# Kernel optimization log

Measured on AMD Instinct MI355X. Metric: run time of the kernel, lower is better.

Reference implementation:

```python
import jax, jax.numpy as jnp
import numpy as np
from functools import partial

B, T_DEC, S_ENC = 64, 30, 31
E, U, V = 128, 256, 32000

def setup_inputs() -> dict:
    key = jax.random.key(0)
    ks = jax.random.split(key, 12)
    sc = lambda *s: 1.0 / np.sqrt(s[0])
    return {
        "inputs": jax.random.randint(ks[0], (B, T_DEC), 0, V, dtype=jnp.int64),
        "memory": jax.random.normal(ks[1], (B, S_ENC, U), jnp.float32),
        "sample_h": jax.random.normal(ks[2], (B, U), jnp.float32),
        "sample_c": jax.random.normal(ks[3], (B, U), jnp.float32),
        "emb_table": jax.random.normal(ks[4], (V, E), jnp.float32) * 0.02,
        "W_k": jax.random.normal(ks[5], (E + U, 4 * U), jnp.float32) * sc(E + U),
        "W_r": jax.random.normal(ks[6], (U, 4 * U), jnp.float32) * sc(U),
        "b_lstm": jnp.zeros((4 * U,), jnp.float32),
        "W_mem": jax.random.normal(ks[7], (U, U), jnp.float32) * sc(U),
        "W_attn": jax.random.normal(ks[8], (2 * U, U), jnp.float32) * sc(2 * U),
        "W_fc": jax.random.normal(ks[9], (U, V), jnp.float32) * sc(U),
        "b_fc": jnp.zeros((V,), jnp.float32),
    }

def _decode(inputs, memory, sample_h, sample_c, emb_table, W_k, W_r, b_lstm,
            W_mem, W_attn, W_fc, b_fc):
    # Luong attention keys: memory_layer(memory), no bias. [B,S,U]
    keys = jnp.einsum('bsu,uv->bsv', memory, W_mem)
    x_emb = emb_table[inputs]                       # [B,T,E]
    xs = jnp.swapaxes(x_emb, 0, 1)                  # [T,B,E]

    def step(carry, x_t):
        h, c, attn = carry
        # AttentionWrapper cell_input_fn: concat(input, prev_attention)
        cell_in = jnp.concatenate([x_t, attn], axis=-1)           # [B,E+U]
        z = cell_in @ W_k + h @ W_r + b_lstm                      # [B,4U]
        i, f, g, o = jnp.split(z, 4, axis=-1)
        c = jax.nn.sigmoid(f) * c + jax.nn.sigmoid(i) * jnp.tanh(g)
        h = jax.nn.sigmoid(o) * jnp.tanh(c)
        # Luong score: query . keys ; memory_sequence_length covers all S, no mask
        score = jnp.einsum('bu,bsu->bs', h, keys)                 # [B,S]
        align = jax.nn.softmax(score, axis=-1)
        context = jnp.einsum('bs,bsu->bu', align, memory)         # [B,U]
        # attention_layer: Dense(U, use_bias=False) on concat(cell_out, context)
        attn = jnp.concatenate([h, context], axis=-1) @ W_attn    # [B,U]
        out_t = attn @ W_fc + b_fc                                # [B,V]
        return (h, c, attn), out_t

    init = (sample_h, sample_c, jnp.zeros((sample_h.shape[0], U), sample_h.dtype))
    _, outs = jax.lax.scan(step, init, xs)          # [T,B,V]
    return jnp.swapaxes(outs, 0, 1)                 # [B,T,V]

def reference(inputs, memory, sample_h, sample_c, emb_table, W_k, W_r, b_lstm,
              W_mem, W_attn, W_fc, b_fc):
    return _decode(inputs, memory, sample_h, sample_c, emb_table, W_k, W_r,
                   b_lstm, W_mem, W_attn, W_fc, b_fc)
```

## Files before the change

kernel.cpp:

```cpp
#include <hip/hip_runtime.h>
#include <hip/hip_bf16.h>
#include <math.h>

constexpr int NB = 64;
constexpr int NT = 30;
constexpr int NS = 31;
constexpr int NE = 128;
constexpr int NU = 256;
constexpr int NV = 32000;
constexpr int NG = 4 * NU;

__device__ __forceinline__ float sigmoidf_(float x) {
    return 1.0f / (1.0f + __expf(-x));
}

__global__ __launch_bounds__(256) void keys_kernel(
    const float* __restrict__ memory, const float* __restrict__ W_mem,
    float* __restrict__ keys) {
    const int row0 = blockIdx.x * 8;
    const int u = threadIdx.x;
    __shared__ float mS[8][NU];
#pragma unroll
    for (int r = 0; r < 8; ++r) mS[r][u] = memory[(row0 + r) * NU + u];
    __syncthreads();
    float acc[8] = {0, 0, 0, 0, 0, 0, 0, 0};
#pragma unroll 4
    for (int v = 0; v < NU; ++v) {
        float w = W_mem[v * NU + u];
#pragma unroll
        for (int r = 0; r < 8; ++r) acc[r] += mS[r][v] * w;
    }
#pragma unroll
    for (int r = 0; r < 8; ++r) keys[(row0 + r) * NU + u] = acc[r];
}

__global__ __launch_bounds__(256) void fuse_wz_kernel(
    const float* __restrict__ W_k,
    const float* __restrict__ W_r,
    const float* __restrict__ W_a,
    float* __restrict__ Wzp)
{
    const int col = blockIdx.x * 256 + threadIdx.x;
    const int rb = blockIdx.y * 8;
    __shared__ float waS[8][NU];
#pragma unroll
    for (int r = 0; r < 8; ++r) waS[r][threadIdx.x] = W_a[(size_t)(rb + r) * NU + threadIdx.x];
    __syncthreads();
    float acc[8] = {};
#pragma unroll 4
    for (int j = 0; j < NU; ++j) {
        float w = W_k[(size_t)(NE + j) * NG + col];
#pragma unroll
        for (int r = 0; r < 8; ++r) acc[r] += waS[r][j] * w;
    }
    const int gate = col >> 8, u = col & 255;
    const int qb = u >> 6, lc = gate * 64 + (u & 63);
#pragma unroll
    for (int r = 0; r < 8; ++r) {
        int i = rb + r;
        float v = acc[r];
        if (i < NU) v += W_r[(size_t)i * NG + col];
        Wzp[(size_t)qb * 512 * 256 + (size_t)i * 256 + lc] = v;
    }
}

__global__ __launch_bounds__(256) void zemb_kernel(
    const int* __restrict__ inputs, const float* __restrict__ emb,
    const float* __restrict__ W_k, const float* __restrict__ b_lstm,
    float* __restrict__ z_emb)
{
    const int col = blockIdx.x * 256 + threadIdx.x;
    const int m0 = blockIdx.y * 8;
    __shared__ float eS[8][NE];
    for (int i = threadIdx.x; i < 8 * NE; i += 256) {
        int r = i >> 7, e = i & 127;
        eS[r][e] = emb[(size_t)inputs[m0 + r] * NE + e];
    }
    __syncthreads();
    float acc[8] = {};
#pragma unroll 4
    for (int e = 0; e < NE; ++e) {
        float w = W_k[(size_t)e * NG + col];
#pragma unroll
        for (int r = 0; r < 8; ++r) acc[r] += eS[r][e] * w;
    }
    float bb = b_lstm[col];
#pragma unroll
    for (int r = 0; r < 8; ++r) z_emb[(size_t)(m0 + r) * NG + col] = acc[r] + bb;
}

__global__ __launch_bounds__(1024, 4) void recurrence_coop(
    const float* __restrict__ z_emb,
    const float* __restrict__ sample_h,
    const float* __restrict__ sample_c,
    const float* __restrict__ Wzp,
    const float* __restrict__ W_r,
    const float* __restrict__ memory,
    const float* __restrict__ keys,
    float* __restrict__ h_all,
    float* __restrict__ ctx_all,
    unsigned* __restrict__ bar)
{
    const int bid = blockIdx.x;
    const int b  = bid & 63;
    const int qb = bid >> 6;
    const int tid = threadIdx.x;

    __shared__ float memS[NS * NU];
    __shared__ float zPart[16 * 256];
    __shared__ float actS[2 * NU];
    __shared__ float scS[32];

    const float* memb = memory + (size_t)b * NS * NU;
    const float* keyb = keys + (size_t)b * NS * NU;
    for (int i = tid; i < NS * NU / 4; i += 1024)
        ((float4*)memS)[i] = ((const float4*)memb)[i];
    if (tid < NU) actS[tid] = sample_h[b * NU + tid];
    float c_reg = (tid < 64) ? sample_c[b * NU + qb * 64 + tid] : 0.0f;

    const int colq = tid & 63;
    const int p    = tid >> 6;
    const int gate = colq >> 4, wq = colq & 15;
    const int ncol = gate * 256 + qb * 64 + wq * 4;
    const float* panel = Wzp + (size_t)qb * 512 * 256;
    const float* zerow = z_emb + (size_t)(b * NT) * NG + ncol;
    unsigned* ctr = bar + b;

    __syncthreads();

    for (int t = 0; t < NT; ++t) {
        {
            float4 acc = (p == 0) ? *(const float4*)(zerow + (size_t)t * NG)
                                  : make_float4(0.f, 0.f, 0.f, 0.f);
            if (t == 0) {
                const float* ap = actS + p * 16;
#pragma unroll
                for (int k = 0; k < 16; ++k) {
                    float a = ap[k];
                    float4 w = *(const float4*)(W_r + (size_t)(p * 16 + k) * NG + ncol);
                    acc.x += a * w.x; acc.y += a * w.y;
                    acc.z += a * w.z; acc.w += a * w.w;
                }
            } else {
                const float* ap = actS + p * 32;
                const float* wp = panel + (size_t)(p * 32) * 256 + colq * 4;
#pragma unroll 8
                for (int k = 0; k < 32; ++k) {
                    float a = ap[k];
                    float4 w = *(const float4*)(wp + k * 256);
                    acc.x += a * w.x; acc.y += a * w.y;
                    acc.z += a * w.z; acc.w += a * w.w;
                }
            }
            *(float4*)(zPart + p * 256 + colq * 4) = acc;
        }
        __syncthreads();

        const size_t m = (size_t)b * NT + t;
        if (tid < 64) {
            float zv[4];
#pragma unroll
            for (int g = 0; g < 4; ++g) {
                float s = 0.f;
#pragma unroll
                for (int q = 0; q < 16; ++q) s += zPart[q * 256 + g * 64 + tid];
                zv[g] = s;
            }
            c_reg = sigmoidf_(zv[1]) * c_reg + sigmoidf_(zv[0]) * tanhf(zv[2]);
            float h = sigmoidf_(zv[3]) * tanhf(c_reg);
            __hip_atomic_store(h_all + m * NU + qb * 64 + tid, h,
                               __ATOMIC_RELAXED, __HIP_MEMORY_SCOPE_AGENT);
        }
        __syncthreads();

        if (tid == 0) {
            __hip_atomic_fetch_add(ctr, 1u, __ATOMIC_RELAXED,
                                   __HIP_MEMORY_SCOPE_AGENT);
            const unsigned tgt = 4u * (unsigned)(t + 1);
            while (__hip_atomic_load(ctr, __ATOMIC_RELAXED,
                                     __HIP_MEMORY_SCOPE_AGENT) < tgt)
                __builtin_amdgcn_s_sleep(2);
        }
        __syncthreads();

        if (tid < NU)
            actS[tid] = __hip_atomic_load(h_all + m * NU + tid,
                                          __ATOMIC_RELAXED,
                                          __HIP_MEMORY_SCOPE_AGENT);
        __syncthreads();

        {
            const int s = tid >> 5, j = tid & 31;
            if (s < NS) {
                float sp = 0.0f;
#pragma unroll
                for (int i = 0; i < 8; ++i)
                    sp += actS[i * 32 + j] * keyb[s * NU + i * 32 + j];
#pragma unroll
                for (int msk = 16; msk; msk >>= 1) sp += __shfl_xor(sp, msk, 32);
                if (j == 0) scS[s] = sp;
            }
        }
        __syncthreads();

        if (tid < NU) {
            float mx = scS[0];
#pragma unroll
            for (int s = 1; s < NS; ++s) mx = fmaxf(mx, scS[s]);
            float sumE = 0.0f, ctx = 0.0f;
#pragma unroll 4
            for (int s = 0; s < NS; ++s) {
                float e = __expf(scS[s] - mx);
                sumE += e;
                ctx += e * memS[s * NU + tid];
            }
            ctx /= sumE;
            actS[NU + tid] = ctx;
            if (qb == 0) ctx_all[m * NU + tid] = ctx;
        }
        __syncthreads();
    }
}

__global__ __launch_bounds__(256) void attn_kernel(
    const float* __restrict__ h_all, const float* __restrict__ ctx_all,
    const float* __restrict__ W_a, float* __restrict__ attn_all)
{
    const int j = threadIdx.x;
    const int m0 = blockIdx.x * 8;
    __shared__ float hS[8][NU], cS[8][NU];
    for (int i = j; i < 8 * NU; i += 256) {
        int r = i >> 8, k = i & 255;
        hS[r][k] = h_all[(size_t)(m0 + r) * NU + k];
        cS[r][k] = ctx_all[(size_t)(m0 + r) * NU + k];
    }
    __syncthreads();
    float acc[8] = {};
#pragma unroll 2
    for (int k = 0; k < NU; ++k) {
        float w1 = W_a[(size_t)k * NU + j];
        float w2 = W_a[(size_t)(NU + k) * NU + j];
#pragma unroll
        for (int r = 0; r < 8; ++r) acc[r] += hS[r][k] * w1 + cS[r][k] * w2;
    }
#pragma unroll
    for (int r = 0; r < 8; ++r) attn_all[(size_t)(m0 + r) * NU + j] = acc[r];
}

constexpr int BM = 128, BN = 128, KC = 32, KTOT = NU;

__global__ __launch_bounds__(256) void out_gemm(
    const float* __restrict__ A,
    const float* __restrict__ Wfc,
    const float* __restrict__ bfc,
    float* __restrict__ out)
{
    const int n0 = blockIdx.x * BN;
    const int m0 = blockIdx.y * BM;
    const int tid = threadIdx.x;
    const int tx = tid & 15, ty = tid >> 4;

    __shared__ float As[KC][BM + 4];
    __shared__ float Bs[KC][BN];

    float acc[2][4][2][4] = {};

    const int kq = tid & 7,  r0 = tid >> 3;
    const int nq = tid & 31, kr0 = tid >> 5;

    float4 aR[4], bR[4];

#pragma unroll
    for (int p = 0; p < 4; ++p)
        aR[p] = *(const float4*)(A + (size_t)(m0 + r0 + p * 32) * KTOT + kq * 4);
#pragma unroll
    for (int p = 0; p < 4; ++p)
        bR[p] = *(const float4*)(Wfc + (size_t)(kr0 + p * 8) * NV + n0 + nq * 4);
#pragma unroll
    for (int p = 0; p < 4; ++p) {
        int r = r0 + p * 32;
        As[kq * 4 + 0][r] = aR[p].x;
        As[kq * 4 + 1][r] = aR[p].y;
        As[kq * 4 + 2][r] = aR[p].z;
        As[kq * 4 + 3][r] = aR[p].w;
        *(float4*)&Bs[kr0 + p * 8][nq * 4] = bR[p];
    }
    __syncthreads();

    for (int kb = 0; kb < KTOT; kb += KC) {
        const bool more = (kb + KC) < KTOT;
        if (more) {
#pragma unroll
            for (int p = 0; p < 4; ++p)
                aR[p] = *(const float4*)(A + (size_t)(m0 + r0 + p * 32) * KTOT + kb + KC + kq * 4);
#pragma unroll
            for (int p = 0; p < 4; ++p)
                bR[p] = *(const float4*)(Wfc + (size_t)(kb + KC + kr0 + p * 8) * NV + n0 + nq * 4);
        }

#pragma unroll 4
        for (int k = 0; k < KC; ++k) {
            float4 a0 = *(const float4*)&As[k][ty * 4];
            float4 a1 = *(const float4*)&As[k][64 + ty * 4];
            float4 b0 = *(const float4*)&Bs[k][tx * 4];
            float4 b1 = *(const float4*)&Bs[k][64 + tx * 4];
            float am[2][4] = {{a0.x, a0.y, a0.z, a0.w}, {a1.x, a1.y, a1.z, a1.w}};
            float bv[2][4] = {{b0.x, b0.y, b0.z, b0.w}, {b1.x, b1.y, b1.z, b1.w}};
#pragma unroll
            for (int im = 0; im < 2; ++im)
#pragma unroll
                for (int i = 0; i < 4; ++i)
#pragma unroll
                    for (int jn = 0; jn < 2; ++jn)
#pragma unroll
                        for (int j = 0; j < 4; ++j)
                            acc[im][i][jn][j] += am[im][i] * bv[jn][j];
        }
        __syncthreads();

        if (more) {
#pragma unroll
            for (int p = 0; p < 4; ++p) {
                int r = r0 + p * 32;
                As[kq * 4 + 0][r] = aR[p].x;
                As[kq * 4 + 1][r] = aR[p].y;
                As[kq * 4 + 2][r] = aR[p].z;
                As[kq * 4 + 3][r] = aR[p].w;
                *(float4*)&Bs[kr0 + p * 8][nq * 4] = bR[p];
            }
            __syncthreads();
        }
    }

    float4 bias[2];
    bias[0] = *(const float4*)(bfc + n0 + tx * 4);
    bias[1] = *(const float4*)(bfc + n0 + 64 + tx * 4);
#pragma unroll
    for (int im = 0; im < 2; ++im)
#pragma unroll
        for (int i = 0; i < 4; ++i) {
            int m = m0 + im * 64 + ty * 4 + i;
#pragma unroll
            for (int jn = 0; jn < 2; ++jn) {
                float4 v;
                float4 bb = bias[jn];
                v.x = acc[im][i][jn][0] + bb.x;
                v.y = acc[im][i][jn][1] + bb.y;
                v.z = acc[im][i][jn][2] + bb.z;
                v.w = acc[im][i][jn][3] + bb.w;
                *(float4*)(out + (size_t)m * NV + n0 + jn * 64 + tx * 4) = v;
            }
        }
}

extern "C" void kernel_launch(void* const* d_in, const int* in_sizes, int n_in,
                              void* d_out, int out_size, void* d_ws, size_t ws_size,
                              hipStream_t stream) {
    const int*   inputs   = (const int*)  d_in[0];
    const float* memory   = (const float*)d_in[1];
    const float* sample_h = (const float*)d_in[2];
    const float* sample_c = (const float*)d_in[3];
    const float* emb      = (const float*)d_in[4];
    const float* W_k      = (const float*)d_in[5];
    const float* W_r      = (const float*)d_in[6];
    const float* b_lstm   = (const float*)d_in[7];
    const float* W_mem    = (const float*)d_in[8];
    const float* W_attn   = (const float*)d_in[9];
    const float* W_fc     = (const float*)d_in[10];
    const float* b_fc     = (const float*)d_in[11];
    float* out = (float*)d_out;

    constexpr size_t SZ_KEYS = (size_t)NB * NS * NU;
    constexpr size_t SZ_WZ   = (size_t)4 * 512 * 256;
    constexpr size_t SZ_ZEMB = (size_t)NB * NT * NG;
    constexpr size_t SZ_ACT  = (size_t)NB * NT * NU;
    float* keys     = (float*)d_ws;
    float* Wzp      = keys + SZ_KEYS;
    float* z_emb    = Wzp + SZ_WZ;
    float* h_all    = z_emb + SZ_ZEMB;
    float* ctx_all  = h_all + SZ_ACT;
    float* attn_all = ctx_all + SZ_ACT;
    unsigned* bar   = (unsigned*)(attn_all + SZ_ACT);

    keys_kernel<<<(NB * NS) / 8, 256, 0, stream>>>(memory, W_mem, keys);
    fuse_wz_kernel<<<dim3(NG / 256, (2 * NU) / 8), 256, 0, stream>>>(W_k, W_r,
                                                                     W_attn, Wzp);
    zemb_kernel<<<dim3(NG / 256, (NB * NT) / 8), 256, 0, stream>>>(inputs, emb,
                                                                   W_k, b_lstm,
                                                                   z_emb);
    hipMemsetAsync(bar, 0, NB * sizeof(unsigned), stream);

    {
        void* kargs[] = {
            (void*)&z_emb, (void*)&sample_h, (void*)&sample_c, (void*)&Wzp,
            (void*)&W_r, (void*)&memory, (void*)&keys, (void*)&h_all,
            (void*)&ctx_all, (void*)&bar
        };
        hipLaunchCooperativeKernel((const void*)recurrence_coop,
                                   dim3(NB * 4), dim3(1024), kargs, 0, stream);
    }

    attn_kernel<<<(NB * NT) / 8, 256, 0, stream>>>(h_all, ctx_all, W_attn,
                                                   attn_all);
    out_gemm<<<dim3(NV / BN, (NB * NT) / BM), 256, 0, stream>>>(attn_all, W_fc,
                                                                b_fc, out);
}
```

Baseline: 1.088 ms.

## Compute output projection with split-bf16 MFMA instead of fp32 SIMT GEMM

Replaces the fp32 output GEMM (1920x256 @ 256x32000) with a bf16 MFMA kernel using a hi/lo split of both operands and three MFMAs per tile, which keeps accuracy close to fp32. W_fc is repacked into a transposed hi/lo bf16 layout on every call, and attn_kernel also writes hi/lo bf16 copies of the activations. Workgroups are remapped across XCDs. The path is taken only when the workspace is large enough, otherwise the old GEMM runs. The per-call repack adds extra traffic over the 32 MB weight.

```diff
diff --git a/kernel.cpp b/kernel.cpp
--- a/kernel.cpp
+++ b/kernel.cpp
@@ -10,8 +10,18 @@
 constexpr int NV = 32000;
 constexpr int NG = 4 * NU;
 
+typedef unsigned short u16;
+typedef __attribute__((ext_vector_type(8))) short bf16x8;
+typedef __attribute__((ext_vector_type(4))) float f32x4;
+
 __device__ __forceinline__ float sigmoidf_(float x) {
     return 1.0f / (1.0f + __expf(-x));
+}
+
+__device__ __forceinline__ u16 rne_bf16(float x) {
+    unsigned u = __float_as_uint(x);
+    unsigned r = u + 0x7fffu + ((u >> 16) & 1u);
+    return (u16)(r >> 16);
 }
 
 __global__ __launch_bounds__(256) void keys_kernel(
@@ -224,7 +234,8 @@
 
 __global__ __launch_bounds__(256) void attn_kernel(
     const float* __restrict__ h_all, const float* __restrict__ ctx_all,
-    const float* __restrict__ W_a, float* __restrict__ attn_all)
+    const float* __restrict__ W_a, float* __restrict__ attn_all,
+    u16* __restrict__ Ahl)
 {
     const int j = threadIdx.x;
     const int m0 = blockIdx.x * 8;
@@ -244,7 +255,120 @@
         for (int r = 0; r < 8; ++r) acc[r] += hS[r][k] * w1 + cS[r][k] * w2;
     }
 #pragma unroll
-    for (int r = 0; r < 8; ++r) attn_all[(size_t)(m0 + r) * NU + j] = acc[r];
+    for (int r = 0; r < 8; ++r) {
+        float a = acc[r];
+        size_t m = (size_t)(m0 + r) * NU + j;
+        attn_all[m] = a;
+        u16 h = rne_bf16(a);
+        float hf = __uint_as_float((unsigned)h << 16);
+        Ahl[m] = h;
+        Ahl[(size_t)NB * NT * NU + m] = rne_bf16(a - hf);
+    }
+}
+
+__global__ __launch_bounds__(256) void wfc_pack(
+    const float* __restrict__ Wfc, u16* __restrict__ Bt)
+{
+    const int n0 = blockIdx.x * 64;
+    const int tid = threadIdx.x;
+    __shared__ __align__(16) u16 tS[64][264];
+
+#pragma unroll
+    for (int part = 0; part < 2; ++part) {
+        for (int kk = 0; kk < 256; kk += 4) {
+            int k = kk + (tid >> 6);
+            int n = tid & 63;
+            float v = Wfc[(size_t)k * NV + n0 + n];
+            u16 h = rne_bf16(v);
+            u16 w = h;
+            if (part) {
+                float hf = __uint_as_float((unsigned)h << 16);
+                w = rne_bf16(v - hf);
+            }
+            tS[n][k] = w;
+        }
+        __syncthreads();
+        {
+            int n = tid >> 2;
+#pragma unroll
+            for (int i = 0; i < 8; ++i) {
+                int c = (tid & 3) + i * 4;
+                *(uint4*)(Bt + (size_t)(n0 + n) * 512 + part * 256 + c * 8) =
+                    *(const uint4*)(&tS[n][c * 8]);
+            }
+        }
+        __syncthreads();
+    }
+}
+
+__global__ __launch_bounds__(256) void out_gemm_mfma(
+    const u16* __restrict__ Ahl,
+    const u16* __restrict__ Bt,
+    const float* __restrict__ bfc,
+    float* __restrict__ out)
+{
+    constexpr int NWG = (NV / 128) * ((NB * NT) / 128);
+    constexpr int qq = NWG / 8, rr = NWG % 8;
+    int bid = blockIdx.x;
+    int xcd = bid & 7, idx = bid >> 3;
+    int wg = (xcd < rr ? xcd * (qq + 1) : rr * (qq + 1) + (xcd - rr) * qq) + idx;
+    const int nt = wg / 15, mt = wg % 15;
+    const int n0 = nt * 128, m0 = mt * 128;
+
+    const int tid = threadIdx.x;
+    const int wave = tid >> 6, lane = tid & 63;
+    const int wm = wave >> 1, wn = wave & 1;
+    const int l15 = lane & 15, lq = lane >> 4;
+
+    constexpr size_t ALOFF = (size_t)NB * NT * NU;
+
+    const u16* arow[4];
+    const u16* brow[4];
+#pragma unroll
+    for (int f = 0; f < 4; ++f) {
+        arow[f] = Ahl + (size_t)(m0 + wm * 64 + f * 16 + l15) * 256 + lq * 8;
+        brow[f] = Bt + (size_t)(n0 + wn * 64 + f * 16 + l15) * 512 + lq * 8;
+    }
+
+    f32x4 acc[4][4] = {};
+
+#pragma unroll
+    for (int kk = 0; kk < 8; ++kk) {
+        bf16x8 ah[4], al[4], bh[4], bl[4];
+#pragma unroll
+        for (int f = 0; f < 4; ++f) {
+            ah[f] = *(const bf16x8*)(arow[f] + kk * 32);
+            al[f] = *(const bf16x8*)(arow[f] + ALOFF + kk * 32);
+            bh[f] = *(const bf16x8*)(brow[f] + kk * 32);
+            bl[f] = *(const bf16x8*)(brow[f] + 256 + kk * 32);
+        }
+#pragma unroll
+        for (int i = 0; i < 4; ++i)
+#pragma unroll
+            for (int j = 0; j < 4; ++j) {
+                acc[i][j] = __builtin_amdgcn_mfma_f32_16x16x32_bf16(
+                    ah[i], bh[j], acc[i][j], 0, 0, 0);
+                acc[i][j] = __builtin_amdgcn_mfma_f32_16x16x32_bf16(
+                    al[i], bh[j], acc[i][j], 0, 0, 0);
+                acc[i][j] = __builtin_amdgcn_mfma_f32_16x16x32_bf16(
+                    ah[i], bl[j], acc[i][j], 0, 0, 0);
+            }
+    }
+
+    float bias[4];
+#pragma unroll
+    for (int j = 0; j < 4; ++j) bias[j] = bfc[n0 + wn * 64 + j * 16 + l15];
+#pragma unroll
+    for (int i = 0; i < 4; ++i) {
+        const int mrow = m0 + wm * 64 + i * 16 + lq * 4;
+#pragma unroll
+        for (int j = 0; j < 4; ++j) {
+            const size_t base = (size_t)mrow * NV + n0 + wn * 64 + j * 16 + l15;
+#pragma unroll
+            for (int rg = 0; rg < 4; ++rg)
+                out[base + (size_t)rg * NV] = acc[i][j][rg] + bias[j];
+        }
+    }
 }
 
 constexpr int BM = 128, BN = 128, KC = 32, KTOT = NU;
@@ -374,13 +498,24 @@
     constexpr size_t SZ_WZ   = (size_t)4 * 512 * 256;
     constexpr size_t SZ_ZEMB = (size_t)NB * NT * NG;
     constexpr size_t SZ_ACT  = (size_t)NB * NT * NU;
+    constexpr size_t SZ_AHL  = SZ_ACT;
+    constexpr size_t SZ_BAR  = 64;
+    constexpr size_t SZ_BT   = (size_t)NV * 512 / 2;
+
     float* keys     = (float*)d_ws;
     float* Wzp      = keys + SZ_KEYS;
     float* z_emb    = Wzp + SZ_WZ;
     float* h_all    = z_emb + SZ_ZEMB;
     float* ctx_all  = h_all + SZ_ACT;
     float* attn_all = ctx_all + SZ_ACT;
-    unsigned* bar   = (unsigned*)(attn_all + SZ_ACT);
+    u16*   Ahl      = (u16*)(attn_all + SZ_ACT);
+    unsigned* bar   = (unsigned*)(attn_all + SZ_ACT + SZ_AHL);
+    float* bt_f     = attn_all + SZ_ACT + SZ_AHL + SZ_BAR;
+    u16*   Bt       = (u16*)bt_f;
+
+    const size_t need_bytes =
+        (SZ_KEYS + SZ_WZ + SZ_ZEMB + 3 * SZ_ACT + SZ_AHL + SZ_BAR + SZ_BT) * 4;
+    const bool use_mfma = ws_size >= need_bytes;
 
     keys_kernel<<<(NB * NS) / 8, 256, 0, stream>>>(memory, W_mem, keys);
     fuse_wz_kernel<<<dim3(NG / 256, (2 * NU) / 8), 256, 0, stream>>>(W_k, W_r,
@@ -388,6 +523,9 @@
     zemb_kernel<<<dim3(NG / 256, (NB * NT) / 8), 256, 0, stream>>>(inputs, emb,
                                                                    W_k, b_lstm,
                                                                    z_emb);
+    if (use_mfma)
+        wfc_pack<<<NV / 64, 256, 0, stream>>>(W_fc, Bt);
+
     hipMemsetAsync(bar, 0, NB * sizeof(unsigned), stream);
 
     {
@@ -401,7 +539,13 @@
     }
 
     attn_kernel<<<(NB * NT) / 8, 256, 0, stream>>>(h_all, ctx_all, W_attn,
-                                                   attn_all);
-    out_gemm<<<dim3(NV / BN, (NB * NT) / BM), 256, 0, stream>>>(attn_all, W_fc,
-                                                                b_fc, out);
-}
+                                                   attn_all, Ahl);
+
+    if (use_mfma) {
+        out_gemm_mfma<<<(NV / 128) * ((NB * NT) / 128), 256, 0, stream>>>(
+            Ahl, Bt, b_fc, out);
+    } else {
+        out_gemm<<<dim3(NV / BN, (NB * NT) / BM), 256, 0, stream>>>(
+            attn_all, W_fc, b_fc, out);
+    }
+}
```

After: 940.4 us. -13.6%, faster.
